# Performance work log

Measured on AMD Instinct MI355X. Metric: run time of the kernel, lower is better.

Reference implementation:

```python
import jax, jax.numpy as jnp
import numpy as np

# --- dims (match init_kwargs / input_specs) ---
B = 2048          # batch
ALEN = 32         # action history length
TP = 16           # prediction horizon
STATE_DIM = 17
ACTION_DIM = 6
TERMS = 33        # s_recon_terms (Fourier ILT terms)
HID = 64          # hidden_units
GRU_H = 32        # hidden_units // 2
OUT = STATE_DIM   # output_dim
LAT = STATE_DIM + 2  # laplace latent dim (state + 2-d action latent)
# Fourier ILT (Dubner-Abate) constants, as in torchlaplace Fourier defaults
ALPHA = 1e-3
TOL = 1e-2        # 10 * alpha
SCALE = 2.0
PI = np.pi


def _gru_layer(x, Wih, Whh, bih, bhh):
    """PyTorch-semantics GRU layer. x: (B, L, D) -> all hidden states (B, L, H)."""
    nb, H = x.shape[0], Whh.shape[1]
    xw = x @ Wih.T + bih  # (B, L, 3H), precomputed input projections

    def step(h, xw_t):
        gh = h @ Whh.T + bhh
        xr, xz, xn = jnp.split(xw_t, 3, axis=-1)
        hr, hz, hn = jnp.split(gh, 3, axis=-1)
        r = jax.nn.sigmoid(xr + hr)
        z = jax.nn.sigmoid(xz + hz)
        n = jnp.tanh(xn + r * hn)
        h = (1.0 - z) * n + z * h
        return h, h

    h0 = jnp.zeros((nb, H), x.dtype)
    _, outs = jax.lax.scan(step, h0, jnp.swapaxes(xw, 0, 1))
    return jnp.swapaxes(outs, 0, 1)


def setup_inputs() -> dict:
    key = jax.random.key(0)
    ks = jax.random.split(key, 20)
    w = lambda k, shape, s=0.1: jax.random.normal(k, shape, jnp.float32) * s
    d = {}
    d["in_batch_obs"] = jax.random.normal(ks[0], (B, STATE_DIM), jnp.float32)
    d["in_batch_action"] = jax.random.normal(ks[1], (B, ALEN, ACTION_DIM), jnp.float32)
    # positive query times (offset avoids t ~ 0 on the Bromwich contour)
    d["ts_pred"] = jax.random.uniform(ks[2], (B, TP), jnp.float32) + 0.1
    # GRU layer 0
    d["gru_Wih0"] = w(ks[3], (3 * GRU_H, ACTION_DIM))
    d["gru_Whh0"] = w(ks[4], (3 * GRU_H, GRU_H))
    d["gru_bih0"] = jnp.zeros((3 * GRU_H,), jnp.float32)
    d["gru_bhh0"] = jnp.zeros((3 * GRU_H,), jnp.float32)
    # GRU layer 1
    d["gru_Wih1"] = w(ks[5], (3 * GRU_H, GRU_H))
    d["gru_Whh1"] = w(ks[6], (3 * GRU_H, GRU_H))
    d["gru_bih1"] = jnp.zeros((3 * GRU_H,), jnp.float32)
    d["gru_bhh1"] = jnp.zeros((3 * GRU_H,), jnp.float32)
    # encoder linear out -> 2-d action latent
    d["enc_Wout"] = w(ks[7], (2, GRU_H))
    d["enc_bout"] = jnp.zeros((2,), jnp.float32)
    # Laplace representation MLP
    d["mlp_W1"] = w(ks[8], (HID, 2 * TERMS + LAT))
    d["mlp_b1"] = jnp.zeros((HID,), jnp.float32)
    d["mlp_W2"] = w(ks[9], (HID, HID))
    d["mlp_b2"] = jnp.zeros((HID,), jnp.float32)
    d["mlp_W3"] = w(ks[10], (2 * OUT * TERMS, HID))
    d["mlp_b3"] = jnp.zeros((2 * OUT * TERMS,), jnp.float32)
    return d


def reference(in_batch_obs, in_batch_action, ts_pred,
              gru_Wih0, gru_Whh0, gru_bih0, gru_bhh0,
              gru_Wih1, gru_Whh1, gru_bih1, gru_bhh1,
              enc_Wout, enc_bout,
              mlp_W1, mlp_b1, mlp_W2, mlp_b2, mlp_W3, mlp_b3):
    # normalize=False branch
    batch_obs = in_batch_obs
    batch_action = in_batch_action / 3.0

    # ---- ReverseGRUEncoder: flip time, 2-layer GRU, last output -> latent(2) ----
    x = batch_action[:, ::-1, :]
    h1 = _gru_layer(x, gru_Wih0, gru_Whh0, gru_bih0, gru_bhh0)
    h2 = _gru_layer(h1, gru_Wih1, gru_Whh1, gru_bih1, gru_bhh1)
    p_action = h2[:, -1, :] @ enc_Wout.T + enc_bout        # (B, 2)
    p = jnp.concatenate([batch_obs, p_action], axis=1)     # (B, LAT)

    # ---- Fourier ILT contour query points s_k = gamma + i*pi*k/T ----
    t = ts_pred                                            # (B, TP)
    Tc = SCALE * t
    gamma = ALPHA - np.log(TOL) / Tc                       # (B, TP)
    k = jnp.arange(TERMS, dtype=t.dtype)                   # (TERMS,)
    s_im = PI * k / Tc[..., None]                          # (B, TP, TERMS)
    s_re = jnp.broadcast_to(gamma[..., None], s_im.shape)
    # Riemann-sphere coordinates of s
    sq = s_re * s_re + s_im * s_im
    theta_s = jnp.arctan2(s_im, s_re)
    phi_s = jnp.arcsin((sq - 1.0) / (sq + 1.0))

    # ---- LaplaceRepresentationFunc (MLP) per (batch, time) point ----
    pt = jnp.broadcast_to(p[:, None, :], (p.shape[0], t.shape[1], LAT))
    inp = jnp.concatenate([theta_s, phi_s, pt], axis=-1)   # (B, TP, 2*TERMS+LAT)
    h = jnp.tanh(inp @ mlp_W1.T + mlp_b1)
    h = jnp.tanh(h @ mlp_W2.T + mlp_b2)
    out = (h @ mlp_W3.T + mlp_b3).reshape(p.shape[0], t.shape[1], 2 * OUT, TERMS)
    theta = jnp.tanh(out[..., :OUT, :]) * PI               # (B, TP, OUT, TERMS)
    phi = jnp.tanh(out[..., OUT:, :]) * (PI / 2.0)         # phi_scale=pi -> (-pi/2, pi/2)

    # ---- inverse stereographic projection: sphere -> complex F(s) ----
    denom = 1.0 - jnp.sin(phi)
    cphi = jnp.cos(phi)
    Fr = jnp.cos(theta) * cphi / denom
    Fi = jnp.sin(theta) * cphi / denom                     # (B, TP, OUT, TERMS)

    # ---- Fourier-series line integral (k=0 term halved), real arithmetic ----
    ang = PI * k * (t / Tc)[..., None]                     # (B, TP, TERMS)
    wk = jnp.where(k == 0, 0.5, 1.0)
    series = wk * (Fr * jnp.cos(ang)[:, :, None, :] - Fi * jnp.sin(ang)[:, :, None, :])
    f = (jnp.exp(gamma * t) / Tc)[..., None] * series.sum(axis=-1)  # (B, TP, OUT)
    return jnp.squeeze(f)


if __name__ == "__main__":
    outs = reference(**setup_inputs())
    print(outs.shape)
```

## Files before the change

kernel.cpp:

```cpp
#include <hip/hip_runtime.h>
#include <math.h>

#define PI_F 3.14159265358979323846f
#define PI_2F 1.57079632679489662f

typedef __attribute__((ext_vector_type(8))) short short8;
typedef __attribute__((ext_vector_type(4))) float f32x4;
#define MFMA16(A,B,C) __builtin_amdgcn_mfma_f32_16x16x32_bf16(A,B,C,0,0,0)
#define SCHED_FENCE() __builtin_amdgcn_sched_barrier(0)

__device__ __forceinline__ float sigm_f(float x) {
    return __fdividef(1.0f, 1.0f + __expf(-x));
}
__device__ __forceinline__ float tanh_f(float x) {
    float xc = fminf(fmaxf(x, -9.0f), 9.0f);
    float e = __expf(2.0f * xc);
    return 1.0f - __fdividef(2.0f, e + 1.0f);
}
__device__ __forceinline__ float atan01(float z) {
    float z2 = z * z;
    float p = fmaf(z2, -0.0117212f, 0.05265332f);
    p = fmaf(z2, p, -0.11643287f);
    p = fmaf(z2, p, 0.19354346f);
    p = fmaf(z2, p, -0.33262347f);
    p = fmaf(z2, p, 0.99997726f);
    return z * p;
}
__device__ __forceinline__ float atan_pos(float x) {
    bool big = x > 1.0f;
    float z = big ? __fdividef(1.0f, x) : x;
    float p = atan01(z);
    return big ? (PI_2F - p) : p;
}
__device__ __forceinline__ unsigned short f2bf(float x) {
    unsigned int u = __float_as_uint(x);
    return (unsigned short)((u + 0x7FFFu + ((u >> 16) & 1u)) >> 16);
}
__device__ __forceinline__ float bf2f(unsigned short h) {
    return __uint_as_float(((unsigned int)h) << 16);
}
__device__ __forceinline__ float lo16f(unsigned int u) { return __uint_as_float(u << 16); }
__device__ __forceinline__ float hi16f(unsigned int u) { return __uint_as_float(u & 0xFFFF0000u); }

__device__ __forceinline__ float lap_term(float at, float ap, int k) {
    float th = tanh_f(at) * PI_F;
    float ph = tanh_f(ap) * (0.5f * PI_F);
    float sph = __sinf(ph), cph = __cosf(ph);
    float rdv = __fdividef(1.0f, 1.0f - sph);
    float tr = __sinf((k & 1) ? th : th + PI_2F);
    float w = (k == 0) ? 0.5f : 1.0f;
    w = ((k + 1) & 2) ? -w : w;
    return w * tr * cph * rdv;
}

__global__ __launch_bounds__(256)
void w3pack_kernel(const float* __restrict__ W3, unsigned short* __restrict__ pk)
{
    int i = blockIdx.x * 256 + threadIdx.x;
    if (i >= 34 * 4096) return;
    int u    = i >> 12;
    int rem  = i & 4095;
    int r    = rem >> 8;
    int rem2 = rem & 255;
    int pl   = rem2 >> 6;
    int s    = rem2 & 63;
    int o = u >> 1, mt = u & 1;
    int row = o * 33 + mt * 16 + r + ((pl >= 2) ? 561 : 0);
    float x = W3[row * 64 + s];
    unsigned short h = f2bf(x);
    pk[i] = (pl & 1) ? f2bf(x - bf2f(h)) : h;
}

__global__ __launch_bounds__(256)
void gru_kernel(const float* __restrict__ act,
                const float* __restrict__ Wih0, const float* __restrict__ Whh0,
                const float* __restrict__ bih0, const float* __restrict__ bhh0,
                const float* __restrict__ Wih1, const float* __restrict__ Whh1,
                const float* __restrict__ bih1, const float* __restrict__ bhh1,
                const float* __restrict__ encW, const float* __restrict__ encb,
                float* __restrict__ p_out)
{
    __shared__ __align__(16) float wih0_l[6 * 128];
    __shared__ __align__(16) unsigned short whh0_p[16 * 32 * 8];
    __shared__ __align__(16) unsigned short wih1_p[16 * 32 * 8];
    __shared__ __align__(16) unsigned short whh1_p[16 * 32 * 8];
    __shared__ float enc_l[64];
    __shared__ __align__(16) float xbuf[4 * 32 * 6];
    __shared__ __align__(16) float hbuf0[4][32];
    __shared__ __align__(16) float hbuf1[4][32];

    const int tid = threadIdx.x;

    for (int idx = tid; idx < 96 * 6; idx += 256) {
        int r = idx / 6, c = idx - r * 6;
        wih0_l[c * 128 + (r & 31) * 4 + (r >> 5)] = Wih0[idx];
    }
    for (int idx = tid; idx < 96 * 32; idx += 256) {
        int r = idx >> 5, c = idx & 31;
        int g = r >> 5, j = r & 31;
        int d = ((c >> 1) * 32 + j) * 8 + g * 2 + (c & 1);
        whh0_p[d] = f2bf(Whh0[idx]);
        wih1_p[d] = f2bf(Wih1[idx]);
        whh1_p[d] = f2bf(Whh1[idx]);
    }
    if (tid < 64) {
        int o = tid >> 5, j = tid & 31;
        enc_l[j * 2 + o] = encW[o * 32 + j];
    }
    {
        const float inv3 = (1.0f / 3.0f);
        int base = blockIdx.x * (4 * 32 * 6);
        for (int idx = tid; idx < 4 * 32 * 6; idx += 256)
            xbuf[idx] = act[base + idx] * inv3;
    }
    __syncthreads();

    const int s = tid >> 6;
    const int l = tid & 63;
    const int j = l & 31;
    const int half = l >> 5;
    const int i0 = half * 16;
    const int sb = half * 8;
    const int j4 = j * 4;
    const int b = blockIdx.x * 4 + s;
    const float z0f = (half == 0) ? 1.0f : 0.0f;

    const float bi0r = z0f * bih0[j], bi0z = z0f * bih0[32 + j], bi0n = z0f * bih0[64 + j];
    const float bh0r = z0f * bhh0[j], bh0z = z0f * bhh0[32 + j], bh0n = z0f * bhh0[64 + j];
    const float bi1r = z0f * bih1[j], bi1z = z0f * bih1[32 + j], bi1n = z0f * bih1[64 + j];
    const float bh1r = z0f * bhh1[j], bh1z = z0f * bhh1[32 + j], bh1n = z0f * bhh1[64 + j];

    float* hb0 = &hbuf0[s][0];
    float* hb1 = &hbuf1[s][0];
    if (!half) { hb0[j] = 0.0f; hb1[j] = 0.0f; }
    float h0 = 0.0f, h1 = 0.0f;
    const float* xs = &xbuf[s * 192];

    for (int t = 0; t < 32; ++t) {
        const float* xt = &xs[(31 - t) * 6];

        float gr0 = bi0r + bh0r, gz0 = bi0z + bh0z, gn0 = bh0n, an = bi0n;
        if (half == 0) {
            #pragma unroll
            for (int d = 0; d < 6; ++d) {
                float xv = xt[d];
                const float4 w = *reinterpret_cast<const float4*>(&wih0_l[d * 128 + j4]);
                gr0 = fmaf(xv, w.x, gr0); gz0 = fmaf(xv, w.y, gz0); an = fmaf(xv, w.z, an);
            }
        }
        {
            float gr1 = 0.0f, gz1 = 0.0f, gn1 = 0.0f;
            #pragma unroll
            for (int m = 0; m < 8; m += 2) {
                const float2 ha = *reinterpret_cast<const float2*>(&hb0[i0 + 2 * m]);
                const float2 hc = *reinterpret_cast<const float2*>(&hb0[i0 + 2 * m + 2]);
                const uint4 wA = *reinterpret_cast<const uint4*>(&whh0_p[((sb + m) * 32 + j) * 8]);
                const uint4 wB = *reinterpret_cast<const uint4*>(&whh0_p[((sb + m + 1) * 32 + j) * 8]);
                gr0 = fmaf(ha.x, lo16f(wA.x), gr0); gr0 = fmaf(ha.y, hi16f(wA.x), gr0);
                gz0 = fmaf(ha.x, lo16f(wA.y), gz0); gz0 = fmaf(ha.y, hi16f(wA.y), gz0);
                gn0 = fmaf(ha.x, lo16f(wA.z), gn0); gn0 = fmaf(ha.y, hi16f(wA.z), gn0);
                gr1 = fmaf(hc.x, lo16f(wB.x), gr1); gr1 = fmaf(hc.y, hi16f(wB.x), gr1);
                gz1 = fmaf(hc.x, lo16f(wB.y), gz1); gz1 = fmaf(hc.y, hi16f(wB.y), gz1);
                gn1 = fmaf(hc.x, lo16f(wB.z), gn1); gn1 = fmaf(hc.y, hi16f(wB.z), gn1);
            }
            float grt = gr0 + gr1; grt += __shfl_xor(grt, 32);
            float gzt = gz0 + gz1; gzt += __shfl_xor(gzt, 32);
            float gnt = gn0 + gn1; gnt += __shfl_xor(gnt, 32);
            float ant = an;        ant += __shfl_xor(ant, 32);
            float r = sigm_f(grt);
            float z = sigm_f(gzt);
            float n = tanh_f(ant + r * gnt);
            h0 = (1.0f - z) * n + z * h0;
            if (!half) hb0[j] = h0;
        }

        {
            float R0 = bi1r + bh1r, Z0 = bi1z + bh1z, aN0 = bi1n, gN0 = bh1n;
            float R1 = 0.0f, Z1 = 0.0f, aN1 = 0.0f, gN1 = 0.0f;
            #pragma unroll
            for (int m = 0; m < 8; m += 2) {
                const float2 ha = *reinterpret_cast<const float2*>(&hb0[i0 + 2 * m]);
                const float2 hc = *reinterpret_cast<const float2*>(&hb0[i0 + 2 * m + 2]);
                const float2 pa = *reinterpret_cast<const float2*>(&hb1[i0 + 2 * m]);
                const float2 pc = *reinterpret_cast<const float2*>(&hb1[i0 + 2 * m + 2]);
                const uint4 aA = *reinterpret_cast<const uint4*>(&wih1_p[((sb + m) * 32 + j) * 8]);
                const uint4 aB = *reinterpret_cast<const uint4*>(&wih1_p[((sb + m + 1) * 32 + j) * 8]);
                const uint4 gA = *reinterpret_cast<const uint4*>(&whh1_p[((sb + m) * 32 + j) * 8]);
                const uint4 gB = *reinterpret_cast<const uint4*>(&whh1_p[((sb + m + 1) * 32 + j) * 8]);
                R0 = fmaf(ha.x, lo16f(aA.x), R0); R0 = fmaf(ha.y, hi16f(aA.x), R0);
                Z0 = fmaf(ha.x, lo16f(aA.y), Z0); Z0 = fmaf(ha.y, hi16f(aA.y), Z0);
                aN0 = fmaf(ha.x, lo16f(aA.z), aN0); aN0 = fmaf(ha.y, hi16f(aA.z), aN0);
                R1 = fmaf(hc.x, lo16f(aB.x), R1); R1 = fmaf(hc.y, hi16f(aB.x), R1);
                Z1 = fmaf(hc.x, lo16f(aB.y), Z1); Z1 = fmaf(hc.y, hi16f(aB.y), Z1);
                aN1 = fmaf(hc.x, lo16f(aB.z), aN1); aN1 = fmaf(hc.y, hi16f(aB.z), aN1);
                R0 = fmaf(pa.x, lo16f(gA.x), R0); R0 = fmaf(pa.y, hi16f(gA.x), R0);
                Z0 = fmaf(pa.x, lo16f(gA.y), Z0); Z0 = fmaf(pa.y, hi16f(gA.y), Z0);
                gN0 = fmaf(pa.x, lo16f(gA.z), gN0); gN0 = fmaf(pa.y, hi16f(gA.z), gN0);
                R1 = fmaf(pc.x, lo16f(gB.x), R1); R1 = fmaf(pc.y, hi16f(gB.x), R1);
                Z1 = fmaf(pc.x, lo16f(gB.y), Z1); Z1 = fmaf(pc.y, hi16f(gB.y), Z1);
                gN1 = fmaf(pc.x, lo16f(gB.z), gN1); gN1 = fmaf(pc.y, hi16f(gB.z), gN1);
            }
            float Rt = R0 + R1;   Rt += __shfl_xor(Rt, 32);
            float Zt = Z0 + Z1;   Zt += __shfl_xor(Zt, 32);
            float aNt = aN0 + aN1; aNt += __shfl_xor(aNt, 32);
            float gNt = gN0 + gN1; gNt += __shfl_xor(gNt, 32);
            float r1 = sigm_f(Rt);
            float z1 = sigm_f(Zt);
            float n1 = tanh_f(aNt + r1 * gNt);
            h1 = (1.0f - z1) * n1 + z1 * h1;
            if (!half) hb1[j] = h1;
        }
    }

    float v0 = h1 * enc_l[j * 2 + 0];
    float v1 = h1 * enc_l[j * 2 + 1];
    #pragma unroll
    for (int off = 16; off > 0; off >>= 1) {
        v0 += __shfl_xor(v0, off, 32);
        v1 += __shfl_xor(v1, off, 32);
    }
    if (l == 0) {
        p_out[b * 2 + 0] = v0 + encb[0];
        p_out[b * 2 + 1] = v1 + encb[1];
    }
}


__device__ __forceinline__ void load_B(const unsigned short* b_hi,
                                       int itm, int ksl, short8& Bh0, short8& Bh1)
{
    const int sw = (itm & 7) << 3;
    Bh0 = *reinterpret_cast<const short8*>(&b_hi[itm * 64 + (ksl ^ sw)]);
    Bh1 = *reinterpret_cast<const short8*>(&b_hi[itm * 64 + ((32 + ksl) ^ sw)]);
}

__device__ __forceinline__ float lap4(f32x4 aT, f32x4 aP, const float* __restrict__ b3,
                                      int rd, int kbase)
{
    float s = 0.0f;
    #pragma unroll
    for (int r = 0; r < 4; ++r)
        s += lap_term(aT[r] + b3[rd + r], aP[r] + b3[rd + r + 561], kbase + r);
    return s;
}

__device__ __forceinline__ float k32_term(const float* __restrict__ W3f,
                                          const float* __restrict__ b3,
                                          const float* __restrict__ h2f,
                                          int o, int l4)
{
    const int rt = o * 33 + 32;
    const float* wtr = W3f + rt * 64;
    const float* wpr = W3f + (rt + 561) * 64;
    float at = b3[rt], ap = b3[rt + 561];
    #pragma unroll
    for (int c = 0; c < 16; ++c) {
        const float4 g4 = *reinterpret_cast<const float4*>(&h2f[c * 256 + l4]);
        at = fmaf(g4.x, wtr[c * 4 + 0], at);
        at = fmaf(g4.y, wtr[c * 4 + 1], at);
        at = fmaf(g4.z, wtr[c * 4 + 2], at);
        at = fmaf(g4.w, wtr[c * 4 + 3], at);
        ap = fmaf(g4.x, wpr[c * 4 + 0], ap);
        ap = fmaf(g4.y, wpr[c * 4 + 1], ap);
        ap = fmaf(g4.z, wpr[c * 4 + 2], ap);
        ap = fmaf(g4.w, wpr[c * 4 + 3], ap);
    }
    return lap_term(at, ap, 32);
}

#define UNIT_G(G, EACC) { \
    short8 Bh0, Bh1; \
    load_B(b_hi, (G) * 16 + lm, ksl, Bh0, Bh1); \
    f32x4 accT = {0.0f, 0.0f, 0.0f, 0.0f}; \
    { \
        const short8 A0 = *reinterpret_cast<const short8*>(au + 0); \
        const short8 A1 = *reinterpret_cast<const short8*>(au + 64); \
        const short8 A2 = *reinterpret_cast<const short8*>(au + 128); \
        const short8 A3 = *reinterpret_cast<const short8*>(au + 192); \
        accT = MFMA16(A0, Bh0, accT); accT = MFMA16(A1, Bh1, accT); \
        accT = MFMA16(A2, Bh0, accT); accT = MFMA16(A3, Bh1, accT); \
    } \
    f32x4 accP = {0.0f, 0.0f, 0.0f, 0.0f}; \
    { \
        const short8 A0 = *reinterpret_cast<const short8*>(au + 256); \
        const short8 A1 = *reinterpret_cast<const short8*>(au + 320); \
        const short8 A2 = *reinterpret_cast<const short8*>(au + 384); \
        const short8 A3 = *reinterpret_cast<const short8*>(au + 448); \
        accP = MFMA16(A0, Bh0, accP); accP = MFMA16(A1, Bh1, accP); \
        accP = MFMA16(A2, Bh0, accP); accP = MFMA16(A3, Bh1, accP); \
    } \
    EACC += lap4(accT, accP, b3, rd, kbase); \
    SCHED_FENCE(); \
}

__global__ __launch_bounds__(512, 4)
void mlp_kernel(const float* __restrict__ obs, const float* __restrict__ ts,
                const float* __restrict__ p_act,
                const float* __restrict__ W1, const float* __restrict__ b1,
                const float* __restrict__ W2, const float* __restrict__ b2,
                const unsigned short* __restrict__ w3pk,
                const float* __restrict__ b3,
                const float* __restrict__ W3f,
                float* __restrict__ out)
{
    __shared__ __align__(16) float h1t[16 * 256];
    __shared__ __align__(16) unsigned short b_hi[64 * 64];
    __shared__ __align__(16) float vtp_lds[33 * 128];
    __shared__ float f_lds[17 * 64];
    __shared__ float f16k32[64];
    __shared__ float scale_lds[64];

    float* h2f = vtp_lds;

    const int tid = threadIdx.x;
    const int wq = __builtin_amdgcn_readfirstlane(tid >> 6);
    const int l = tid & 63;
    const int l4 = l * 4;
    const int item = blockIdx.x * 64 + l;
    const int b = item >> 4;
    const int obase = wq * 8;

    const float t = ts[item];
    const float rTc = __fdividef(0.5f, t);
    const float gamma = 0.001f + 4.6051701859880913680f * rTc;

    if (wq == 0) scale_lds[l] = __expf(gamma * t) * rTc;

    const float gam2 = gamma * gamma;
    const float rg = __fdividef(1.0f, gamma);
    const float pirTc = PI_F * rTc;

    for (int k = wq; k < 33; k += 8) {
        float sim = (float)k * pirTc;
        float vth = atan_pos(sim * rg);
        float sq = fmaf(sim, sim, gam2);
        float vph = fmaf(-2.0f, atan01(rsqrtf(sq)), PI_2F);
        vtp_lds[k * 128 + (l << 1) + 0] = vth;
        vtp_lds[k * 128 + (l << 1) + 1] = vph;
    }
    __syncthreads();

    {
        float acc[8];
        #pragma unroll
        for (int oo = 0; oo < 8; ++oo) acc[oo] = b1[obase + oo];
        const float* w1b = W1 + obase * 85;

        for (int k = 0; k < 33; ++k) {
            const float2 tp = *reinterpret_cast<const float2*>(&vtp_lds[k * 128 + (l << 1)]);
            #pragma unroll
            for (int oo = 0; oo < 8; ++oo) {
                acc[oo] = fmaf(tp.x, w1b[oo * 85 + k], acc[oo]);
                acc[oo] = fmaf(tp.y, w1b[oo * 85 + 33 + k], acc[oo]);
            }
        }
        #pragma unroll
        for (int j = 0; j < 19; ++j) {
            float pv = (j < 17) ? obs[b * 17 + j] : p_act[b * 2 + (j - 17)];
            #pragma unroll
            for (int oo = 0; oo < 8; ++oo)
                acc[oo] = fmaf(pv, w1b[oo * 85 + 66 + j], acc[oo]);
        }
        #pragma unroll
        for (int oo = 0; oo < 8; ++oo) {
            int o = obase + oo;
            h1t[(o >> 2) * 256 + l4 + (o & 3)] = tanh_f(acc[oo]);
        }
    }
    __syncthreads();

    {
        float acc[8];
        #pragma unroll
        for (int oo = 0; oo < 8; ++oo) acc[oo] = b2[obase + oo];
        #pragma unroll
        for (int c = 0; c < 16; ++c) {
            const float4 g4 = *reinterpret_cast<const float4*>(&h1t[c * 256 + l4]);
            #pragma unroll
            for (int oo = 0; oo < 8; ++oo) {
                const float* wr = W2 + (obase + oo) * 64 + c * 4;
                acc[oo] = fmaf(g4.x, wr[0], acc[oo]);
                acc[oo] = fmaf(g4.y, wr[1], acc[oo]);
                acc[oo] = fmaf(g4.z, wr[2], acc[oo]);
                acc[oo] = fmaf(g4.w, wr[3], acc[oo]);
            }
        }
        const int sw = (l & 7) << 3;
        #pragma unroll
        for (int p = 0; p < 4; ++p) {
            float v0 = tanh_f(acc[2 * p + 0]);
            float v1 = tanh_f(acc[2 * p + 1]);
            int o0 = obase + 2 * p;
            h2f[((o0 + 0) >> 2) * 256 + l4 + ((o0 + 0) & 3)] = v0;
            h2f[((o0 + 1) >> 2) * 256 + l4 + ((o0 + 1) & 3)] = v1;
            unsigned short h0 = f2bf(v0), h1v = f2bf(v1);
            int ksw = o0 ^ sw;
            *reinterpret_cast<unsigned int*>(&b_hi[l * 64 + ksw]) =
                (unsigned int)h0 | ((unsigned int)h1v << 16);
        }
    }
    __syncthreads();

    {
        const int lm = l & 15;
        const int lq = l >> 4;
        const int ksl = lq * 8;
        const char* apk = (const char*)w3pk;
        const int lane_off = lm * 512 + lq * 16;

        #pragma unroll 1
        for (int oo2 = 0; oo2 < 2; ++oo2) {
            const int o = wq * 2 + oo2;
            const float k32t = k32_term(W3f, b3, h2f, o, l4);
            float e0 = 0.0f, e1 = 0.0f, e2 = 0.0f, e3 = 0.0f;

            #pragma unroll 1
            for (int mt = 0; mt < 2; ++mt) {
                const char* au = apk + ((o * 2 + mt) << 13) + lane_off;
                const int rd = o * 33 + mt * 16 + lq * 4;
                const int kbase = mt * 16 + lq * 4;

                UNIT_G(0, e0)
                UNIT_G(1, e1)
                UNIT_G(2, e2)
                UNIT_G(3, e3)
            }
            e0 += __shfl_xor(e0, 16); e0 += __shfl_xor(e0, 32);
            e1 += __shfl_xor(e1, 16); e1 += __shfl_xor(e1, 32);
            e2 += __shfl_xor(e2, 16); e2 += __shfl_xor(e2, 32);
            e3 += __shfl_xor(e3, 16); e3 += __shfl_xor(e3, 32);
            float tot = (lq == 0) ? e0 : (lq == 1) ? e1 : (lq == 2) ? e2 : e3;
            f_lds[o * 64 + l] = tot + k32t;
        }

        if (wq < 4) {
            const int g = wq;
            float facc = 0.0f;
            #pragma unroll 1
            for (int mt = 0; mt < 2; ++mt) {
                const char* au = apk + ((16 * 2 + mt) << 13) + lane_off;
                const int rd = 16 * 33 + mt * 16 + lq * 4;
                const int kbase = mt * 16 + lq * 4;
                UNIT_G(g, facc)
            }
            facc += __shfl_xor(facc, 16);
            facc += __shfl_xor(facc, 32);
            if (l < 16) f_lds[16 * 64 + g * 16 + l] = facc;
        } else if (wq == 4) {
            f16k32[l] = k32_term(W3f, b3, h2f, 16, l4);
        }
    }
    __syncthreads();

    const int base_item = blockIdx.x * 64;
    for (int idx = tid; idx < 64 * 17; idx += 512) {
        const int li = idx / 17;
        const int o  = idx - li * 17;
        float v = f_lds[o * 64 + li];
        if (o == 16) v += f16k32[li];
        out[(base_item + li) * 17 + o] = v * scale_lds[li];
    }
}

extern "C" void kernel_launch(void* const* d_in, const int* in_sizes, int n_in,
                              void* d_out, int out_size, void* d_ws, size_t ws_size,
                              hipStream_t stream) {
    (void)in_sizes; (void)n_in; (void)out_size; (void)ws_size;
    const float* obs  = (const float*)d_in[0];
    const float* act  = (const float*)d_in[1];
    const float* ts   = (const float*)d_in[2];
    const float* Wih0 = (const float*)d_in[3];
    const float* Whh0 = (const float*)d_in[4];
    const float* bih0 = (const float*)d_in[5];
    const float* bhh0 = (const float*)d_in[6];
    const float* Wih1 = (const float*)d_in[7];
    const float* Whh1 = (const float*)d_in[8];
    const float* bih1 = (const float*)d_in[9];
    const float* bhh1 = (const float*)d_in[10];
    const float* encW = (const float*)d_in[11];
    const float* encb = (const float*)d_in[12];
    const float* W1   = (const float*)d_in[13];
    const float* b1   = (const float*)d_in[14];
    const float* W2   = (const float*)d_in[15];
    const float* b2   = (const float*)d_in[16];
    const float* W3   = (const float*)d_in[17];
    const float* b3   = (const float*)d_in[18];
    float* o_ptr  = (float*)d_out;

    float* p_act = (float*)d_ws;
    unsigned short* w3pk = (unsigned short*)((char*)d_ws + 16384);

    w3pack_kernel<<<dim3((34 * 4096 + 255) / 256), dim3(256), 0, stream>>>(W3, w3pk);
    gru_kernel<<<dim3(512), dim3(256), 0, stream>>>(
        act, Wih0, Whh0, bih0, bhh0, Wih1, Whh1, bih1, bhh1, encW, encb, p_act);
    mlp_kernel<<<dim3(512), dim3(512), 0, stream>>>(
        obs, ts, p_act, W1, b1, W2, b2, w3pk, b3, W3, o_ptr);
}
```

Baseline: 116.7 us.

## Redistribute final-layer MFMA and Laplace terms across all waves per output

The final MLP layer is repartitioned so that each output channel is handled by all 8 waves together: each wave computes one (row-group, M-tile) MFMA block and writes the raw accumulators to LDS. All waves then evaluate the Laplace series terms for 4 k-values each, and a reduction over waves adds the partial sums into f_lds. The k=32 terms are precomputed by all threads up front, which removes the imbalanced tail where only half the waves handled output 16. The cost is three block-wide barriers per output channel (51 in total) plus extra LDS round trips, in exchange for better load balance and removal of the shuffle reductions.

```diff
diff --git a/kernel.cpp b/kernel.cpp
--- a/kernel.cpp
+++ b/kernel.cpp
@@ -7,7 +7,6 @@
 typedef __attribute__((ext_vector_type(8))) short short8;
 typedef __attribute__((ext_vector_type(4))) float f32x4;
 #define MFMA16(A,B,C) __builtin_amdgcn_mfma_f32_16x16x32_bf16(A,B,C,0,0,0)
-#define SCHED_FENCE() __builtin_amdgcn_sched_barrier(0)
 
 __device__ __forceinline__ float sigm_f(float x) {
     return __fdividef(1.0f, 1.0f + __expf(-x));
@@ -226,24 +225,6 @@
 }
 
 
-__device__ __forceinline__ void load_B(const unsigned short* b_hi,
-                                       int itm, int ksl, short8& Bh0, short8& Bh1)
-{
-    const int sw = (itm & 7) << 3;
-    Bh0 = *reinterpret_cast<const short8*>(&b_hi[itm * 64 + (ksl ^ sw)]);
-    Bh1 = *reinterpret_cast<const short8*>(&b_hi[itm * 64 + ((32 + ksl) ^ sw)]);
-}
-
-__device__ __forceinline__ float lap4(f32x4 aT, f32x4 aP, const float* __restrict__ b3,
-                                      int rd, int kbase)
-{
-    float s = 0.0f;
-    #pragma unroll
-    for (int r = 0; r < 4; ++r)
-        s += lap_term(aT[r] + b3[rd + r], aP[r] + b3[rd + r + 561], kbase + r);
-    return s;
-}
-
 __device__ __forceinline__ float k32_term(const float* __restrict__ W3f,
                                           const float* __restrict__ b3,
                                           const float* __restrict__ h2f,
@@ -268,31 +249,6 @@
     return lap_term(at, ap, 32);
 }
 
-#define UNIT_G(G, EACC) { \
-    short8 Bh0, Bh1; \
-    load_B(b_hi, (G) * 16 + lm, ksl, Bh0, Bh1); \
-    f32x4 accT = {0.0f, 0.0f, 0.0f, 0.0f}; \
-    { \
-        const short8 A0 = *reinterpret_cast<const short8*>(au + 0); \
-        const short8 A1 = *reinterpret_cast<const short8*>(au + 64); \
-        const short8 A2 = *reinterpret_cast<const short8*>(au + 128); \
-        const short8 A3 = *reinterpret_cast<const short8*>(au + 192); \
-        accT = MFMA16(A0, Bh0, accT); accT = MFMA16(A1, Bh1, accT); \
-        accT = MFMA16(A2, Bh0, accT); accT = MFMA16(A3, Bh1, accT); \
-    } \
-    f32x4 accP = {0.0f, 0.0f, 0.0f, 0.0f}; \
-    { \
-        const short8 A0 = *reinterpret_cast<const short8*>(au + 256); \
-        const short8 A1 = *reinterpret_cast<const short8*>(au + 320); \
-        const short8 A2 = *reinterpret_cast<const short8*>(au + 384); \
-        const short8 A3 = *reinterpret_cast<const short8*>(au + 448); \
-        accP = MFMA16(A0, Bh0, accP); accP = MFMA16(A1, Bh1, accP); \
-        accP = MFMA16(A2, Bh0, accP); accP = MFMA16(A3, Bh1, accP); \
-    } \
-    EACC += lap4(accT, accP, b3, rd, kbase); \
-    SCHED_FENCE(); \
-}
-
 __global__ __launch_bounds__(512, 4)
 void mlp_kernel(const float* __restrict__ obs, const float* __restrict__ ts,
                 const float* __restrict__ p_act,
@@ -305,12 +261,14 @@
 {
     __shared__ __align__(16) float h1t[16 * 256];
     __shared__ __align__(16) unsigned short b_hi[64 * 64];
-    __shared__ __align__(16) float vtp_lds[33 * 128];
+    __shared__ __align__(16) float pool[33 * 128];
     __shared__ float f_lds[17 * 64];
-    __shared__ float f16k32[64];
     __shared__ float scale_lds[64];
 
-    float* h2f = vtp_lds;
+    float* h2f  = pool;
+    float* at_l = pool;
+    float* ap_l = pool + 32 * 65;
+    float* part_l = h1t;
 
     const int tid = threadIdx.x;
     const int wq = __builtin_amdgcn_readfirstlane(tid >> 6);
@@ -335,8 +293,8 @@
         float vth = atan_pos(sim * rg);
         float sq = fmaf(sim, sim, gam2);
         float vph = fmaf(-2.0f, atan01(rsqrtf(sq)), PI_2F);
-        vtp_lds[k * 128 + (l << 1) + 0] = vth;
-        vtp_lds[k * 128 + (l << 1) + 1] = vph;
+        pool[k * 128 + (l << 1) + 0] = vth;
+        pool[k * 128 + (l << 1) + 1] = vph;
     }
     __syncthreads();
 
@@ -347,7 +305,7 @@
         const float* w1b = W1 + obase * 85;
 
         for (int k = 0; k < 33; ++k) {
-            const float2 tp = *reinterpret_cast<const float2*>(&vtp_lds[k * 128 + (l << 1)]);
+            const float2 tp = *reinterpret_cast<const float2*>(&pool[k * 128 + (l << 1)]);
             #pragma unroll
             for (int oo = 0; oo < 8; ++oo) {
                 acc[oo] = fmaf(tp.x, w1b[oo * 85 + k], acc[oo]);
@@ -385,6 +343,7 @@
                 acc[oo] = fmaf(g4.w, wr[3], acc[oo]);
             }
         }
+        __syncthreads();
         const int sw = (l & 7) << 3;
         #pragma unroll
         for (int p = 0; p < 4; ++p) {
@@ -401,64 +360,85 @@
     }
     __syncthreads();
 
+    for (int idx = tid; idx < 17 * 64; idx += 512) {
+        int o = __builtin_amdgcn_readfirstlane(idx >> 6);
+        f_lds[idx] = k32_term(W3f, b3, h2f, o, (idx & 63) * 4);
+    }
+    __syncthreads();
+
     {
         const int lm = l & 15;
         const int lq = l >> 4;
         const int ksl = lq * 8;
+        const int g  = wq & 3;
+        const int mt = wq >> 2;
         const char* apk = (const char*)w3pk;
         const int lane_off = lm * 512 + lq * 16;
+        const int itm = g * 16 + lm;
+        const int sw = (itm & 7) << 3;
+        const unsigned short* bb = &b_hi[itm * 64];
 
         #pragma unroll 1
-        for (int oo2 = 0; oo2 < 2; ++oo2) {
-            const int o = wq * 2 + oo2;
-            const float k32t = k32_term(W3f, b3, h2f, o, l4);
-            float e0 = 0.0f, e1 = 0.0f, e2 = 0.0f, e3 = 0.0f;
-
-            #pragma unroll 1
-            for (int mt = 0; mt < 2; ++mt) {
+        for (int o = 0; o < 17; ++o) {
+            {
                 const char* au = apk + ((o * 2 + mt) << 13) + lane_off;
-                const int rd = o * 33 + mt * 16 + lq * 4;
-                const int kbase = mt * 16 + lq * 4;
-
-                UNIT_G(0, e0)
-                UNIT_G(1, e1)
-                UNIT_G(2, e2)
-                UNIT_G(3, e3)
-            }
-            e0 += __shfl_xor(e0, 16); e0 += __shfl_xor(e0, 32);
-            e1 += __shfl_xor(e1, 16); e1 += __shfl_xor(e1, 32);
-            e2 += __shfl_xor(e2, 16); e2 += __shfl_xor(e2, 32);
-            e3 += __shfl_xor(e3, 16); e3 += __shfl_xor(e3, 32);
-            float tot = (lq == 0) ? e0 : (lq == 1) ? e1 : (lq == 2) ? e2 : e3;
-            f_lds[o * 64 + l] = tot + k32t;
-        }
-
-        if (wq < 4) {
-            const int g = wq;
-            float facc = 0.0f;
-            #pragma unroll 1
-            for (int mt = 0; mt < 2; ++mt) {
-                const char* au = apk + ((16 * 2 + mt) << 13) + lane_off;
-                const int rd = 16 * 33 + mt * 16 + lq * 4;
-                const int kbase = mt * 16 + lq * 4;
-                UNIT_G(g, facc)
-            }
-            facc += __shfl_xor(facc, 16);
-            facc += __shfl_xor(facc, 32);
-            if (l < 16) f_lds[16 * 64 + g * 16 + l] = facc;
-        } else if (wq == 4) {
-            f16k32[l] = k32_term(W3f, b3, h2f, 16, l4);
-        }
-    }
-    __syncthreads();
+                const short8 Bh0 = *reinterpret_cast<const short8*>(bb + (ksl ^ sw));
+                const short8 Bh1 = *reinterpret_cast<const short8*>(bb + ((32 + ksl) ^ sw));
+                f32x4 accT = {0.0f, 0.0f, 0.0f, 0.0f};
+                {
+                    const short8 A0 = *reinterpret_cast<const short8*>(au + 0);
+                    const short8 A1 = *reinterpret_cast<const short8*>(au + 64);
+                    const short8 A2 = *reinterpret_cast<const short8*>(au + 128);
+                    const short8 A3 = *reinterpret_cast<const short8*>(au + 192);
+                    accT = MFMA16(A0, Bh0, accT); accT = MFMA16(A1, Bh1, accT);
+                    accT = MFMA16(A2, Bh0, accT); accT = MFMA16(A3, Bh1, accT);
+                }
+                f32x4 accP = {0.0f, 0.0f, 0.0f, 0.0f};
+                {
+                    const short8 A0 = *reinterpret_cast<const short8*>(au + 256);
+                    const short8 A1 = *reinterpret_cast<const short8*>(au + 320);
+                    const short8 A2 = *reinterpret_cast<const short8*>(au + 384);
+                    const short8 A3 = *reinterpret_cast<const short8*>(au + 448);
+                    accP = MFMA16(A0, Bh0, accP); accP = MFMA16(A1, Bh1, accP);
+                    accP = MFMA16(A2, Bh0, accP); accP = MFMA16(A3, Bh1, accP);
+                }
+                #pragma unroll
+                for (int r = 0; r < 4; ++r) {
+                    const int kk = mt * 16 + lq * 4 + r;
+                    at_l[kk * 65 + itm] = accT[r];
+                    ap_l[kk * 65 + itm] = accP[r];
+                }
+            }
+            __syncthreads();
+
+            {
+                float part = 0.0f;
+                #pragma unroll
+                for (int r = 0; r < 4; ++r) {
+                    const int kk = wq * 4 + r;
+                    float at = at_l[kk * 65 + l] + b3[o * 33 + kk];
+                    float ap = ap_l[kk * 65 + l] + b3[o * 33 + kk + 561];
+                    part += lap_term(at, ap, kk);
+                }
+                part_l[wq * 64 + l] = part;
+            }
+            __syncthreads();
+
+            if (tid < 64) {
+                float s = 0.0f;
+                #pragma unroll
+                for (int q = 0; q < 8; ++q) s += part_l[q * 64 + tid];
+                f_lds[o * 64 + tid] += s;
+            }
+            __syncthreads();
+        }
+    }
 
     const int base_item = blockIdx.x * 64;
     for (int idx = tid; idx < 64 * 17; idx += 512) {
         const int li = idx / 17;
         const int o  = idx - li * 17;
-        float v = f_lds[o * 64 + li];
-        if (o == 16) v += f16k32[li];
-        out[(base_item + li) * 17 + o] = v * scale_lds[li];
+        out[(base_item + li) * 17 + o] = f_lds[o * 64 + li] * scale_lds[li];
     }
 }
 
```

Measured after the change: 140.5 us. 1.2x slower.
